# Kernel tuning notes

Measured on AMD Instinct MI355X. Metric: run time of the kernel, lower is better.

Reference implementation:

```python
import jax, jax.numpy as jnp
import numpy as np
import math

NUM_GRIDS = 128
INPUT_DIM = 128
OUTPUT_DIM = 128
BATCH = 8192
INIT_SCALE = 0.1


def _borders_cdf_grid(n_chunks):
    # inverse Laplace CDF grid borders, exactly as in the torch module
    def inv(u):
        return np.log(2.0 * u) if u <= 0.5 else -np.log(2.0 * (1.0 - u))
    cs = 1.0 / n_chunks
    b = [inv(i * cs) for i in range(1, n_chunks)]
    left = b[0] - (b[1] - b[0])
    right = b[-1] + (b[-1] - b[-2])
    return np.array([left] + b + [right], dtype=np.float32)  # [n_chunks+1]


def setup_inputs() -> dict:
    key = jax.random.key(0)
    kx, kp = jax.random.split(key)
    x = jax.random.normal(kx, (INPUT_DIM, BATCH), dtype=jnp.float32)
    s = INIT_SCALE / math.sqrt(INPUT_DIM)
    func_parameter = jax.random.uniform(
        kp, (NUM_GRIDS + 1, OUTPUT_DIM, INPUT_DIM), dtype=jnp.float32,
        minval=-s, maxval=s)
    borders = jnp.asarray(_borders_cdf_grid(NUM_GRIDS))
    inverse_chunk_lengths = 1.0 / (borders[1:] - borders[:-1])  # [NUM_GRIDS]
    return {"x": x, "func_parameter": func_parameter,
            "borders": borders, "inverse_chunk_lengths": inverse_chunk_lengths}


def reference(x, func_parameter, borders, inverse_chunk_lengths):
    # x: [I, B]; func_parameter: [G+1, O, I]
    G = borders.shape[0] - 1
    I = x.shape[0]
    # Laplace CDF: R -> [0, 1]
    exp_na = jnp.exp(-jnp.abs(x))
    cdf = jnp.where(x > 0, 1.0 - 0.5 * exp_na, 0.5 * exp_na)
    # bucketize on uniform CDF grid (truncation == floor since cdf*G >= 0)
    idx = jnp.clip((cdf * G).astype(jnp.int32), 0, G - 1)        # [I, B]
    idx_next = jnp.clip(idx + 1, 0, G)                           # [I, B]
    left = borders[idx]                                          # [I, B]
    inv_len = inverse_chunk_lengths[idx]                         # [I, B]
    d = (x - left) * inv_len                                     # [I, B]
    # gather per-input-dim parameter rows: val[i, b, o] = P[idx[i,b], o, i]
    Pt = jnp.transpose(func_parameter, (2, 0, 1))                # [I, G+1, O]
    rows = jnp.arange(I)[:, None]                                # [I, 1]
    val_l = Pt[rows, idx]                                        # [I, B, O]
    val_r = Pt[rows, idx_next]                                   # [I, B, O]
    out = ((1.0 - d)[..., None] * val_l + d[..., None] * val_r).sum(axis=0)  # [B, O]
    return out.T                                                 # [O, B]
```

## Files before the change

kernel.cpp:

```cpp
#include <hip/hip_runtime.h>
#include <cstdint>


#define NG 128
#define NI 128
#define NO 128
#define NB 8192
#define WO 4
#define PH 8
#define NPH (NI / PH)

using half2v = __attribute__((ext_vector_type(2))) _Float16;

__device__ inline uint32_t pack_f16x2(float lo, float hi) {
    _Float16 hl = (_Float16)lo, hh = (_Float16)hi;
    return (uint32_t)__builtin_bit_cast(unsigned short, hl) |
           ((uint32_t)__builtin_bit_cast(unsigned short, hh) << 16);
}

__global__ __launch_bounds__(256) void build_q(const float* __restrict__ P,
                                               uint32_t* __restrict__ Q2) {
    __shared__ float lp[32][129];
    __shared__ float ln[32][129];
    const int g  = blockIdx.x >> 2;
    const int o0 = (blockIdx.x & 3) * 32;
    const int t  = threadIdx.x;
    #pragma unroll
    for (int p = 0; p < 16; ++p) {
        int e = p * 256 + t;
        int ol = e >> 7, i = e & 127;
        lp[ol][i] = P[(size_t)(g * NO + o0 + ol) * NI + i];
        ln[ol][i] = P[(size_t)((g + 1) * NO + o0 + ol) * NI + i];
    }
    __syncthreads();
    #pragma unroll
    for (int p = 0; p < 4; ++p) {
        int e = p * 256 + t;
        int sl = e >> 7, i = e & 127;
        uint32_t r[4];
        #pragma unroll
        for (int ow = 0; ow < 4; ++ow) {
            float pl = lp[sl * 4 + ow][i];
            float dd = ln[sl * 4 + ow][i] - pl;
            r[ow] = pack_f16x2(pl, dd);
        }
        int s = (o0 >> 2) + sl;
        *(uint4*)(Q2 + ((size_t)(s * NI + i) * NG + g) * 4) =
            make_uint4(r[0], r[1], r[2], r[3]);
    }
}

__global__ __launch_bounds__(256) void build_t(const float* __restrict__ x,
                                               const float* __restrict__ borders,
                                               const float* __restrict__ icl,
                                               uint32_t* __restrict__ T) {
    const int e0 = (blockIdx.x * 256 + threadIdx.x) * 4;
    const float4 xv = *(const float4*)(x + e0);
    uint32_t r[4];
    const float xs[4] = {xv.x, xv.y, xv.z, xv.w};
    #pragma unroll
    for (int k = 0; k < 4; ++k) {
        float v = xs[k];
        float ea = __expf(-fabsf(v));
        float cdf = v > 0.f ? 1.f - 0.5f * ea : 0.5f * ea;
        int idx = (int)(cdf * 128.f);
        idx = idx > 127 ? 127 : idx;
        float d = (v - borders[idx]) * icl[idx];
        _Float16 hd = (_Float16)d;
        r[k] = ((uint32_t)idx << 4) |
               ((uint32_t)__builtin_bit_cast(unsigned short, hd) << 16);
    }
    *(uint4*)(T + e0) = make_uint4(r[0], r[1], r[2], r[3]);
}

__global__ __launch_bounds__(1024) void main_k(const uint32_t* __restrict__ Q2,
                                               const uint32_t* __restrict__ T,
                                               float* __restrict__ out) {
    __shared__ uint32_t slab[2][PH][NG * WO];
    const int t    = threadIdx.x;
    const int bx   = blockIdx.x;
    const int s    = bx & 31;
    const int bblk = (bx >> 5) << 10;
    const int bme  = bblk + t;
    const uint32_t* Qs = Q2 + (size_t)s * NI * NG * WO;

    float a0 = 0.f, a1 = 0.f, a2 = 0.f, a3 = 0.f;

    uint32_t treg[PH];
    {
        uint4 q0 = *(const uint4*)(Qs + (size_t)t * 4);
        #pragma unroll
        for (int il = 0; il < PH; ++il)
            treg[il] = T[(size_t)il * NB + bme];
        ((uint4*)&slab[0][0][0])[t] = q0;
    }
    __syncthreads();

    #pragma unroll
    for (int p = 0; p < NPH; ++p) {
        const int cur = p & 1;
        uint32_t tnxt[PH];
        uint4 qnxt;
        if (p < NPH - 1) {
            qnxt = *(const uint4*)(Qs + (size_t)(p + 1) * (PH * NG * WO) +
                                   (size_t)t * 4);
            #pragma unroll
            for (int il = 0; il < PH; ++il)
                tnxt[il] = T[(size_t)((p + 1) * PH + il) * NB + bme];
        }
        #pragma unroll
        for (int il = 0; il < PH; ++il) {
            uint32_t tw  = treg[il];
            uint32_t off = tw & 0xFFFFu;
            uint32_t w2b = (tw & 0xFFFF0000u) | 0x3C00u;
            uint4 q = *(const uint4*)((const char*)&slab[cur][il][0] + off);
            half2v w2 = __builtin_bit_cast(half2v, w2b);
            a0 = __builtin_amdgcn_fdot2(__builtin_bit_cast(half2v, q.x), w2, a0, false);
            a1 = __builtin_amdgcn_fdot2(__builtin_bit_cast(half2v, q.y), w2, a1, false);
            a2 = __builtin_amdgcn_fdot2(__builtin_bit_cast(half2v, q.z), w2, a2, false);
            a3 = __builtin_amdgcn_fdot2(__builtin_bit_cast(half2v, q.w), w2, a3, false);
        }
        if (p < NPH - 1) {
            ((uint4*)&slab[cur ^ 1][0][0])[t] = qnxt;
            #pragma unroll
            for (int il = 0; il < PH; ++il)
                treg[il] = tnxt[il];
            __syncthreads();
        }
    }

    size_t ob = (size_t)(s * 4) * NB + bme;
    __builtin_nontemporal_store(a0, out + ob);
    __builtin_nontemporal_store(a1, out + ob + NB);
    __builtin_nontemporal_store(a2, out + ob + 2 * (size_t)NB);
    __builtin_nontemporal_store(a3, out + ob + 3 * (size_t)NB);
}

extern "C" void kernel_launch(void* const* d_in, const int* in_sizes, int n_in,
                              void* d_out, int out_size, void* d_ws, size_t ws_size,
                              hipStream_t stream) {
    const float* x       = (const float*)d_in[0];
    const float* P       = (const float*)d_in[1];
    const float* borders = (const float*)d_in[2];
    const float* icl     = (const float*)d_in[3];
    float* out = (float*)d_out;

    uint32_t* Q2 = (uint32_t*)d_ws;
    uint32_t* T  = Q2 + (size_t)NO * NI * NG;

    hipLaunchKernelGGL(build_q, dim3(NG * 4), dim3(256), 0, stream, P, Q2);
    hipLaunchKernelGGL(build_t, dim3(NI * NB / 1024), dim3(256), 0, stream,
                       x, borders, icl, T);
    hipLaunchKernelGGL(main_k, dim3((NB / 1024) * 32), dim3(1024), 0, stream,
                       Q2, T, out);
}
```

Baseline: 93.72 us.

## Merge Q and T preprocessing kernels and store pairwise weights in T

Merges the parameter-packing and input-bucketizing preprocessing kernels into a single launch that branches on block index. The packed parameters now hold (left, right) values, and T stores a separate offset word plus packed (1-d, d) weights. The main loop no longer needs bit masking to build the weight pair, and it is no longer unrolled, which shrinks code size. In exchange, T doubles in size (8 bytes per element), adding global read traffic in the main kernel and write traffic in preprocessing.

```diff
diff --git a/kernel.cpp b/kernel.cpp
--- a/kernel.cpp
+++ b/kernel.cpp
@@ -9,6 +9,7 @@
 #define WO 4
 #define PH 8
 #define NPH (NI / PH)
+#define PHW (PH * NG * WO)
 
 using half2v = __attribute__((ext_vector_type(2))) _Float16;
 
@@ -18,63 +19,62 @@
            ((uint32_t)__builtin_bit_cast(unsigned short, hh) << 16);
 }
 
-__global__ __launch_bounds__(256) void build_q(const float* __restrict__ P,
-                                               uint32_t* __restrict__ Q2) {
-    __shared__ float lp[32][129];
-    __shared__ float ln[32][129];
-    const int g  = blockIdx.x >> 2;
-    const int o0 = (blockIdx.x & 3) * 32;
+__global__ __launch_bounds__(256) void build_qt(const float* __restrict__ P,
+                                                const float* __restrict__ x,
+                                                const float* __restrict__ borders,
+                                                const float* __restrict__ icl,
+                                                uint32_t* __restrict__ Q2,
+                                                uint2* __restrict__ T2) {
+    const int bx = blockIdx.x;
     const int t  = threadIdx.x;
-    #pragma unroll
-    for (int p = 0; p < 16; ++p) {
-        int e = p * 256 + t;
-        int ol = e >> 7, i = e & 127;
-        lp[ol][i] = P[(size_t)(g * NO + o0 + ol) * NI + i];
-        ln[ol][i] = P[(size_t)((g + 1) * NO + o0 + ol) * NI + i];
-    }
-    __syncthreads();
-    #pragma unroll
-    for (int p = 0; p < 4; ++p) {
-        int e = p * 256 + t;
-        int sl = e >> 7, i = e & 127;
-        uint32_t r[4];
+    if (bx < 512) {
+        __shared__ float lp[32][129];
+        __shared__ float ln[32][129];
+        const int g  = bx >> 2;
+        const int o0 = (bx & 3) * 32;
         #pragma unroll
-        for (int ow = 0; ow < 4; ++ow) {
-            float pl = lp[sl * 4 + ow][i];
-            float dd = ln[sl * 4 + ow][i] - pl;
-            r[ow] = pack_f16x2(pl, dd);
+        for (int p = 0; p < 16; ++p) {
+            int e = p * 256 + t;
+            int ol = e >> 7, i = e & 127;
+            lp[ol][i] = P[(size_t)(g * NO + o0 + ol) * NI + i];
+            ln[ol][i] = P[(size_t)((g + 1) * NO + o0 + ol) * NI + i];
         }
-        int s = (o0 >> 2) + sl;
-        *(uint4*)(Q2 + ((size_t)(s * NI + i) * NG + g) * 4) =
-            make_uint4(r[0], r[1], r[2], r[3]);
+        __syncthreads();
+        #pragma unroll
+        for (int p = 0; p < 4; ++p) {
+            int e = p * 256 + t;
+            int sl = e >> 7, i = e & 127;
+            uint32_t r[4];
+            #pragma unroll
+            for (int ow = 0; ow < 4; ++ow)
+                r[ow] = pack_f16x2(lp[sl * 4 + ow][i], ln[sl * 4 + ow][i]);
+            int s = (o0 >> 2) + sl;
+            *(uint4*)(Q2 + ((size_t)(s * NI + i) * NG + g) * 4) =
+                make_uint4(r[0], r[1], r[2], r[3]);
+        }
+    } else {
+        const int e0 = ((bx - 512) * 256 + t) * 4;
+        const float4 xv = *(const float4*)(x + e0);
+        uint2 r[4];
+        const float xs[4] = {xv.x, xv.y, xv.z, xv.w};
+        #pragma unroll
+        for (int k = 0; k < 4; ++k) {
+            float v = xs[k];
+            float ea = __expf(-fabsf(v));
+            float cdf = v > 0.f ? 1.f - 0.5f * ea : 0.5f * ea;
+            int idx = (int)(cdf * 128.f);
+            idx = idx > 127 ? 127 : idx;
+            float d = (v - borders[idx]) * icl[idx];
+            r[k].x = (uint32_t)idx << 4;
+            r[k].y = pack_f16x2(1.f - d, d);
+        }
+        *(uint4*)(T2 + e0)     = make_uint4(r[0].x, r[0].y, r[1].x, r[1].y);
+        *(uint4*)(T2 + e0 + 2) = make_uint4(r[2].x, r[2].y, r[3].x, r[3].y);
     }
 }
 
-__global__ __launch_bounds__(256) void build_t(const float* __restrict__ x,
-                                               const float* __restrict__ borders,
-                                               const float* __restrict__ icl,
-                                               uint32_t* __restrict__ T) {
-    const int e0 = (blockIdx.x * 256 + threadIdx.x) * 4;
-    const float4 xv = *(const float4*)(x + e0);
-    uint32_t r[4];
-    const float xs[4] = {xv.x, xv.y, xv.z, xv.w};
-    #pragma unroll
-    for (int k = 0; k < 4; ++k) {
-        float v = xs[k];
-        float ea = __expf(-fabsf(v));
-        float cdf = v > 0.f ? 1.f - 0.5f * ea : 0.5f * ea;
-        int idx = (int)(cdf * 128.f);
-        idx = idx > 127 ? 127 : idx;
-        float d = (v - borders[idx]) * icl[idx];
-        _Float16 hd = (_Float16)d;
-        r[k] = ((uint32_t)idx << 4) |
-               ((uint32_t)__builtin_bit_cast(unsigned short, hd) << 16);
-    }
-    *(uint4*)(T + e0) = make_uint4(r[0], r[1], r[2], r[3]);
-}
-
 __global__ __launch_bounds__(1024) void main_k(const uint32_t* __restrict__ Q2,
-                                               const uint32_t* __restrict__ T,
+                                               const uint2* __restrict__ T2,
                                                float* __restrict__ out) {
     __shared__ uint32_t slab[2][PH][NG * WO];
     const int t    = threadIdx.x;
@@ -83,48 +83,46 @@
     const int bblk = (bx >> 5) << 10;
     const int bme  = bblk + t;
     const uint32_t* Qs = Q2 + (size_t)s * NI * NG * WO;
+    const uint2* Tb = T2 + bme;
 
     float a0 = 0.f, a1 = 0.f, a2 = 0.f, a3 = 0.f;
+    uint2 tc[PH];
 
-    uint32_t treg[PH];
     {
         uint4 q0 = *(const uint4*)(Qs + (size_t)t * 4);
         #pragma unroll
         for (int il = 0; il < PH; ++il)
-            treg[il] = T[(size_t)il * NB + bme];
+            tc[il] = Tb[(size_t)il * NB];
         ((uint4*)&slab[0][0][0])[t] = q0;
     }
     __syncthreads();
 
-    #pragma unroll
+    #pragma unroll 1
     for (int p = 0; p < NPH; ++p) {
         const int cur = p & 1;
-        uint32_t tnxt[PH];
-        uint4 qnxt;
+        uint2 tn[PH];
+        uint4 qn;
         if (p < NPH - 1) {
-            qnxt = *(const uint4*)(Qs + (size_t)(p + 1) * (PH * NG * WO) +
-                                   (size_t)t * 4);
+            qn = *(const uint4*)(Qs + (size_t)(p + 1) * PHW + (size_t)t * 4);
             #pragma unroll
             for (int il = 0; il < PH; ++il)
-                tnxt[il] = T[(size_t)((p + 1) * PH + il) * NB + bme];
+                tn[il] = Tb[(size_t)((p + 1) * PH + il) * NB];
         }
         #pragma unroll
         for (int il = 0; il < PH; ++il) {
-            uint32_t tw  = treg[il];
-            uint32_t off = tw & 0xFFFFu;
-            uint32_t w2b = (tw & 0xFFFF0000u) | 0x3C00u;
-            uint4 q = *(const uint4*)((const char*)&slab[cur][il][0] + off);
-            half2v w2 = __builtin_bit_cast(half2v, w2b);
+            uint2 tv = tc[il];
+            uint4 q = *(const uint4*)((const char*)&slab[cur][il][0] + tv.x);
+            half2v w2 = __builtin_bit_cast(half2v, tv.y);
             a0 = __builtin_amdgcn_fdot2(__builtin_bit_cast(half2v, q.x), w2, a0, false);
             a1 = __builtin_amdgcn_fdot2(__builtin_bit_cast(half2v, q.y), w2, a1, false);
             a2 = __builtin_amdgcn_fdot2(__builtin_bit_cast(half2v, q.z), w2, a2, false);
             a3 = __builtin_amdgcn_fdot2(__builtin_bit_cast(half2v, q.w), w2, a3, false);
         }
         if (p < NPH - 1) {
-            ((uint4*)&slab[cur ^ 1][0][0])[t] = qnxt;
+            ((uint4*)&slab[cur ^ 1][0][0])[t] = qn;
             #pragma unroll
             for (int il = 0; il < PH; ++il)
-                treg[il] = tnxt[il];
+                tc[il] = tn[il];
             __syncthreads();
         }
     }
@@ -146,11 +144,10 @@
     float* out = (float*)d_out;
 
     uint32_t* Q2 = (uint32_t*)d_ws;
-    uint32_t* T  = Q2 + (size_t)NO * NI * NG;
+    uint2*    T2 = (uint2*)(Q2 + (size_t)NO * NI * NG);
 
-    hipLaunchKernelGGL(build_q, dim3(NG * 4), dim3(256), 0, stream, P, Q2);
-    hipLaunchKernelGGL(build_t, dim3(NI * NB / 1024), dim3(256), 0, stream,
-                       x, borders, icl, T);
+    hipLaunchKernelGGL(build_qt, dim3(512 + NI * NB / 1024), dim3(256), 0,
+                       stream, P, x, borders, icl, Q2, T2);
     hipLaunchKernelGGL(main_k, dim3((NB / 1024) * 32), dim3(1024), 0, stream,
-                       Q2, T, out);
+                       Q2, T2, out);
 }
```

Result: slower. 102.5 us (+9.4%).
